# Kernel tuning notes

Hardware: AMD Instinct MI355X
Metric: run time of the kernel (lower is better)

Reference implementation:

```python
import jax, jax.numpy as jnp
import numpy as np

D_MODEL = 1024
NUM_HEADS = 16
D_K = D_MODEL // NUM_HEADS  # 64
THETA = 10000.0


def setup_inputs() -> dict:
    key = jax.random.key(0)
    k_x, k_q, k_k, k_v, k_o = jax.random.split(key, 5)
    B, S = 2, 2048
    std = (2.0 / (D_MODEL + D_MODEL)) ** 0.5
    x = jax.random.normal(k_x, (B, S, D_MODEL), dtype=jnp.float32)
    Wq = std * jax.random.truncated_normal(k_q, -3.0, 3.0, (D_MODEL, D_MODEL), dtype=jnp.float32)
    Wk = std * jax.random.truncated_normal(k_k, -3.0, 3.0, (D_MODEL, D_MODEL), dtype=jnp.float32)
    Wv = std * jax.random.truncated_normal(k_v, -3.0, 3.0, (D_MODEL, D_MODEL), dtype=jnp.float32)
    Wo = std * jax.random.truncated_normal(k_o, -3.0, 3.0, (D_MODEL, D_MODEL), dtype=jnp.float32)
    return {"x": x, "Wq": Wq, "Wk": Wk, "Wv": Wv, "Wo": Wo}


def _apply_rope(t, cos, sin):
    # t: [B, H, S, d_k]; cos/sin: [S, d_k//2] broadcast over B, H
    tr = t.reshape(*t.shape[:-1], D_K // 2, 2)
    t1, t2 = tr[..., 0], tr[..., 1]
    r1 = t1 * cos - t2 * sin
    r2 = t1 * sin + t2 * cos
    return jnp.stack([r1, r2], axis=-1).reshape(t.shape)


def reference(x, Wq, Wk, Wv, Wo):
    B, S, D = x.shape
    H, dk = NUM_HEADS, D_K
    # projections (no bias): y = x @ W.T
    Q = (x @ Wq.T).reshape(B, S, H, dk).transpose(0, 2, 1, 3)  # [B,H,S,dk]
    K = (x @ Wk.T).reshape(B, S, H, dk).transpose(0, 2, 1, 3)
    V = (x @ Wv.T).reshape(B, S, H, dk).transpose(0, 2, 1, 3)
    # RoPE angles for positions 0..S-1
    pos = jnp.arange(S, dtype=jnp.float32)[:, None]            # [S,1]
    freqs = 1.0 / (THETA ** (jnp.arange(0, dk, 2, dtype=jnp.float32) / dk))  # [dk/2]
    angles = pos * freqs[None, :]                              # [S, dk/2]
    cos, sin = jnp.cos(angles), jnp.sin(angles)
    Q = _apply_rope(Q, cos, sin)
    K = _apply_rope(K, cos, sin)
    # causal scaled dot-product attention
    scores = jnp.einsum("bhqd,bhkd->bhqk", Q, K) / jnp.sqrt(jnp.float32(dk))
    causal = jnp.tril(jnp.ones((S, S), dtype=bool))
    scores = jnp.where(causal, scores, -jnp.inf)
    probs = jax.nn.softmax(scores, axis=-1)
    attn = jnp.einsum("bhqk,bhkd->bhqd", probs, V)             # [B,H,S,dk]
    attn = attn.transpose(0, 2, 1, 3).reshape(B, S, H * dk)
    return attn @ Wo.T
```

## Files before the change

### kernel.cpp

```cpp
#include <hip/hip_runtime.h>
#include <hip/hip_bf16.h>

typedef __bf16 bf16;
typedef __bf16 bf16x8 __attribute__((ext_vector_type(8)));
typedef float f32x4 __attribute__((ext_vector_type(4)));

#define MFMA16(A, B, C) __builtin_amdgcn_mfma_f32_16x16x32_bf16((A), (B), (C), 0, 0, 0)

static __device__ __forceinline__ void gload16(const bf16* g, bf16* l) {
    __builtin_amdgcn_global_load_lds((const __attribute__((address_space(1))) void*)g,
                                     (__attribute__((address_space(3))) void*)l, 16, 0, 0);
}

__global__ void detect_kernel(const void* w, int* flag) {
    float v = (float)((const bf16*)w)[threadIdx.x];
    unsigned long long bad = __ballot(!(fabsf(v) < 1.0f));
    if (threadIdx.x == 0) *flag = bad ? 1 : 0;
}

__global__ __launch_bounds__(256) void convert_all(const void* x, const void* w0,
                                                   const void* w1, const void* w2,
                                                   const void* w3, bf16* xb, bf16* b0,
                                                   bf16* b1, bf16* b2, bf16* b3,
                                                   const int* flagp) {
    if (*flagp == 0) return;
    int id = (blockIdx.x * 256 + threadIdx.x) * 4;
    const int XN = 1 << 22;
    const float* src;
    bf16* dst;
    int off;
    if (id < XN) {
        src = (const float*)x; dst = xb; off = id;
    } else {
        int r = id - XN;
        int wi = r >> 20;
        off = r & ((1 << 20) - 1);
        src = (const float*)(wi == 0 ? w0 : wi == 1 ? w1 : wi == 2 ? w2 : w3);
        dst = (wi == 0 ? b0 : wi == 1 ? b1 : wi == 2 ? b2 : b3);
    }
    float4 v = *(const float4*)(src + off);
    bf16 o[4] = {(bf16)v.x, (bf16)v.y, (bf16)v.z, (bf16)v.w};
    *(uint2*)(dst + off) = *(uint2*)o;
}

template <int MODE>
__global__ __launch_bounds__(256, 3) void gemm_nt(const void* rawA, const bf16* convA,
                                                  const void* rW0, const bf16* cW0,
                                                  const void* rW1, const bf16* cW1,
                                                  const void* rW2, const bf16* cW2,
                                                  bf16* Qo, bf16* Ko, bf16* Vt,
                                                  float* p0, float* p1,
                                                  const int* flagp) {
    const int K = 1024;
    __shared__ __attribute__((aligned(16))) bf16 lsA[2][128 * 32];
    __shared__ __attribute__((aligned(16))) bf16 lsB[2][128 * 32];
    const int flag = *flagp;
    const bf16* A = flag ? convA : (const bf16*)rawA;
    int tensor, n0, m0, ks;
    const bf16* W;
    if (MODE == 0) {
        tensor = blockIdx.x >> 3;
        n0 = (blockIdx.x & 7) * 128;
        m0 = blockIdx.y * 128;
        ks = 0;
        W = tensor == 0 ? (flag ? cW0 : (const bf16*)rW0)
          : tensor == 1 ? (flag ? cW1 : (const bf16*)rW1)
                        : (flag ? cW2 : (const bf16*)rW2);
    } else {
        const int bid = blockIdx.x;
        ks = bid & 1;
        const int slot = bid >> 1;
        m0 = (slot & 31) * 128;
        n0 = (slot >> 5) * 128;
        tensor = 0;
        W = flag ? cW0 : (const bf16*)rW0;
    }
    const int t = threadIdx.x;
    const int w = t >> 6, lane = t & 63;
    const int wr = w >> 1, wc = w & 1;
    const int llo = lane & 15, quad = lane >> 4;
    const int sel = (llo >> 1) & 3;

    f32x4 acc[4][4] = {};

    auto stage = [&](int k0, int buf) {
#pragma unroll
        for (int j = 0; j < 2; ++j) {
            int c = j * 256 + t;
            int row = c >> 2, pos = c & 3;
            int g = pos ^ ((row >> 1) & 3);
            gload16(A + (size_t)(m0 + row) * K + k0 + g * 8, &lsA[buf][c * 8]);
        }
#pragma unroll
        for (int j = 0; j < 2; ++j) {
            int c = j * 256 + t;
            int row = c >> 2, pos = c & 3;
            int g = pos ^ ((row >> 1) & 3);
            gload16(W + (size_t)(n0 + row) * K + k0 + g * 8, &lsB[buf][c * 8]);
        }
    };

    auto compute = [&](int buf) {
        bf16x8 a[4], bb[4];
#pragma unroll
        for (int mi = 0; mi < 4; ++mi) {
            int r = wr * 64 + mi * 16 + llo;
            a[mi] = *(const bf16x8*)&lsA[buf][r * 32 + ((quad ^ sel) * 8)];
        }
#pragma unroll
        for (int ni = 0; ni < 4; ++ni) {
            int r = wc * 64 + ni * 16 + llo;
            bb[ni] = *(const bf16x8*)&lsB[buf][r * 32 + ((quad ^ sel) * 8)];
        }
#pragma unroll
        for (int mi = 0; mi < 4; ++mi)
#pragma unroll
            for (int ni = 0; ni < 4; ++ni)
                acc[mi][ni] = MFMA16(a[mi], bb[ni], acc[mi][ni]);
    };

    const int kbase = (MODE == 1) ? ks * 512 : 0;
    const int NIT = (MODE == 1) ? 16 : 32;

    stage(kbase, 0);
    for (int it = 0; it < NIT; it += 2) {
        __syncthreads();
        stage(kbase + (it + 1) * 32, 1);
        compute(0);
        __syncthreads();
        if (it + 2 < NIT) stage(kbase + (it + 2) * 32, 0);
        compute(1);
    }

#pragma unroll
    for (int mi = 0; mi < 4; ++mi)
#pragma unroll
        for (int ni = 0; ni < 4; ++ni)
#pragma unroll
            for (int r = 0; r < 4; ++r) {
                int row = m0 + wr * 64 + mi * 16 + quad * 4 + r;
                int col = n0 + wc * 64 + ni * 16 + llo;
                float v = acc[mi][ni][r];
                if (MODE == 1) {
                    float* dst = ks ? p1 : p0;
                    dst[(size_t)row * 1024 + col] = v;
                } else if (tensor == 2) {
                    int b = row >> 11, s = row & 2047;
                    Vt[((size_t)b * 1024 + col) * 2048 + s] = (bf16)v;
                } else {
                    int d = col & 63, s = row & 2047;
                    float partner = __shfl_xor(v, 1);
                    float freq = exp2f((float)(d >> 1) * -0.4152410118609203f);
                    float rev = (float)s * freq * 0.15915494309189535f;
                    rev -= floorf(rev);
                    float sn = __builtin_amdgcn_sinf(rev);
                    float cs = __builtin_amdgcn_cosf(rev);
                    float outv = v * cs + partner * sn * ((d & 1) ? 1.0f : -1.0f);
                    bf16* dst = (tensor == 0) ? Qo : Ko;
                    dst[(size_t)row * 1024 + col] = (bf16)outv;
                }
            }
}

__global__ __launch_bounds__(256) void reduce_out(const float* p0, const float* p1,
                                                  void* dout, const int* flagp) {
    int i = (blockIdx.x * 256 + threadIdx.x) * 4;
    float4 a = *(const float4*)(p0 + i);
    float4 b = *(const float4*)(p1 + i);
    float4 s = {a.x + b.x, a.y + b.y, a.z + b.z, a.w + b.w};
    if (*flagp) {
        *(float4*)((float*)dout + i) = s;
    } else {
        bf16 o[4] = {(bf16)s.x, (bf16)s.y, (bf16)s.z, (bf16)s.w};
        *(uint2*)((bf16*)dout + i) = *(uint2*)o;
    }
}

__global__ __launch_bounds__(256, 3) void attn_kernel(const bf16* __restrict__ Q,
                                                      const bf16* __restrict__ Kr,
                                                      const bf16* __restrict__ Vt,
                                                      bf16* __restrict__ O,
                                                      bf16* __restrict__ Opart,
                                                      float* __restrict__ lws) {
    __shared__ __attribute__((aligned(16))) bf16 lsK[2][64 * 64];
    __shared__ __attribute__((aligned(16))) bf16 lsV[2][64 * 64];
    __shared__ __attribute__((aligned(16))) bf16 lsP[4][32 * 64];
    const int blk = blockIdx.x;
    int ib, bh, s, tt0, tt1;
    bool split;
    if (blk < 512) {
        split = true;
        s = blk >> 8;
        int c = blk & 255;
        ib = 15 - (c >> 5);
        bh = c & 31;
        tt0 = s ? (ib + 1) : 0;
        tt1 = s ? (2 * ib + 1) : ib;
    } else {
        split = false;
        s = 0;
        int c = blk - 512;
        ib = c >> 5;
        bh = c & 31;
        tt0 = 0;
        tt1 = 2 * ib + 1;
    }
    const int b = bh >> 4, h = bh & 15;
    const int t = threadIdx.x, w = t >> 6, lane = t & 63;
    const int llo = lane & 15, quad = lane >> 4;
    const int q0w = ib * 128 + w * 32;

    bf16x8 aQ[2][2];
#pragma unroll
    for (int qi = 0; qi < 2; ++qi) {
        const size_t qb =
            ((size_t)(b * 2048 + q0w + qi * 16 + llo)) * 1024 + h * 64 + quad * 8;
        aQ[qi][0] = *(const bf16x8*)&Q[qb];
        aQ[qi][1] = *(const bf16x8*)&Q[qb + 32];
    }

    f32x4 o[2][4] = {};
    float lpart[2] = {0.f, 0.f};
    const float SC = 0.18033688011112042f;
    const int qlane0 = q0w + llo;

    const int srow8 = lane >> 3;
    const int sc = (lane & 7) ^ srow8;

    auto stage = [&](int tt, int buf) {
        const int kv0 = tt * 64;
#pragma unroll
        for (int jj = 0; jj < 2; ++jj) {
            int seg = w + jj * 4;
            int rowk = seg * 8 + srow8;
            gload16(&Kr[((size_t)(b * 2048 + kv0 + rowk)) * 1024 + h * 64 + sc * 8],
                    &lsK[buf][seg * 512 + lane * 8]);
            gload16(&Vt[((size_t)(b * 1024 + h * 64 + rowk)) * 2048 + kv0 + sc * 8],
                    &lsV[buf][seg * 512 + lane * 8]);
        }
    };

    stage(tt0, 0);

    for (int tt = tt0; tt <= tt1; ++tt) {
        const int cur = (tt - tt0) & 1;
        const int kv0 = tt * 64;
        __syncthreads();
        if (tt + 1 <= tt1) stage(tt + 1, cur ^ 1);

        if (kv0 <= q0w + 31) {
            bf16x8 kf[4][2];
#pragma unroll
            for (int half = 0; half < 4; ++half) {
                int rk = half * 16 + llo;
                kf[half][0] = *(const bf16x8*)&lsK[cur][rk * 64 + ((quad ^ (rk & 7)) * 8)];
                kf[half][1] =
                    *(const bf16x8*)&lsK[cur][rk * 64 + (((quad + 4) ^ (rk & 7)) * 8)];
            }
            bf16x8 vf[2][4];
#pragma unroll
            for (int kc = 0; kc < 2; ++kc)
#pragma unroll
                for (int g = 0; g < 4; ++g) {
                    int rv = g * 16 + llo;
                    int cg = kc * 4 + quad;
                    vf[kc][g] =
                        *(const bf16x8*)&lsV[cur][rv * 64 + ((cg ^ (rv & 7)) * 8)];
                }

            const bool need_mask = (kv0 + 63 >= q0w);
#pragma unroll
            for (int qi = 0; qi < 2; ++qi) {
                const int q = qlane0 + qi * 16;
                const int prow = qi * 16 + llo;
#pragma unroll
                for (int half = 0; half < 4; ++half) {
                    f32x4 z = {};
                    z = MFMA16(kf[half][0], aQ[qi][0], z);
                    z = MFMA16(kf[half][1], aQ[qi][1], z);
                    union { bf16 hh[4]; uint2 uu; } pk;
                    if (need_mask) {
                        int kvb = kv0 + half * 16 + quad * 4;
#pragma unroll
                        for (int r = 0; r < 4; ++r) {
                            float e = (kvb + r <= q) ? z[r] * SC : -INFINITY;
                            float p = __builtin_amdgcn_exp2f(e);
                            lpart[qi] += p;
                            pk.hh[r] = (bf16)p;
                        }
                    } else {
#pragma unroll
                        for (int r = 0; r < 4; ++r) {
                            float p = __builtin_amdgcn_exp2f(z[r] * SC);
                            lpart[qi] += p;
                            pk.hh[r] = (bf16)p;
                        }
                    }
                    int cw = 2 * half + (quad >> 1);
                    *(uint2*)&lsP[w][prow * 64 + ((cw ^ (llo & 7)) * 8) + (quad & 1) * 4] =
                        pk.uu;
                }
            }
            __builtin_amdgcn_wave_barrier();
#pragma unroll
            for (int qi = 0; qi < 2; ++qi) {
                const int prow = qi * 16 + llo;
#pragma unroll
                for (int kc = 0; kc < 2; ++kc) {
                    int cr = 4 * kc + quad;
                    bf16x8 aP =
                        *(const bf16x8*)&lsP[w][prow * 64 + ((cr ^ (llo & 7)) * 8)];
#pragma unroll
                    for (int g = 0; g < 4; ++g) o[qi][g] = MFMA16(aP, vf[kc][g], o[qi][g]);
                }
            }
            __builtin_amdgcn_wave_barrier();
        }
    }

    float lfull[2];
#pragma unroll
    for (int qi = 0; qi < 2; ++qi) {
        float l = lpart[qi];
        l += __shfl_xor(l, 16);
        l += __shfl_xor(l, 32);
        lfull[qi] = l;
    }

    if (split) {
        const int slotw = ((ib - 8) * 32 + bh) * 2 + s;
        bf16* op = Opart + (size_t)slotw * 8192;
#pragma unroll
        for (int qi = 0; qi < 2; ++qi) {
#pragma unroll
            for (int r = 0; r < 4; ++r) {
                int row_in = w * 32 + qi * 16 + quad * 4 + r;
#pragma unroll
                for (int g = 0; g < 4; ++g)
                    op[row_in * 64 + g * 16 + llo] = (bf16)o[qi][g][r];
            }
            if (quad == 0) lws[slotw * 128 + w * 32 + qi * 16 + llo] = lfull[qi];
        }
    } else {
#pragma unroll
        for (int qi = 0; qi < 2; ++qi)
#pragma unroll
            for (int r = 0; r < 4; ++r) {
                float l = __shfl(lfull[qi], (lane & 48) | (quad * 4 + r));
                float inv = 1.f / l;
                int q = q0w + qi * 16 + quad * 4 + r;
                size_t ob = ((size_t)(b * 2048 + q)) * 1024 + h * 64;
#pragma unroll
                for (int g = 0; g < 4; ++g)
                    O[ob + g * 16 + llo] = (bf16)(o[qi][g][r] * inv);
            }
    }
}

__global__ __launch_bounds__(256) void combine_kernel(const bf16* __restrict__ Opart,
                                                      const float* __restrict__ lws,
                                                      bf16* __restrict__ AO) {
    int id = blockIdx.x * 256 + threadIdx.x;
    int d = id & 63;
    int h = (id >> 6) & 15;
    int qoff = (id >> 10) & 1023;
    int b = id >> 20;
    int ib8 = qoff >> 7;
    int q_in = qoff & 127;
    int slot = (ib8 * 32 + (b * 16 + h)) * 2;
    size_t base = (size_t)slot * 8192 + q_in * 64 + d;
    float o0 = (float)Opart[base];
    float o1 = (float)Opart[base + 8192];
    float l = lws[slot * 128 + q_in] + lws[(slot + 1) * 128 + q_in];
    int q = 1024 + qoff;
    AO[((size_t)(b * 2048 + q)) * 1024 + h * 64 + d] = (bf16)((o0 + o1) / l);
}

extern "C" void kernel_launch(void* const* d_in, const int* in_sizes, int n_in,
                              void* d_out, int out_size, void* d_ws, size_t ws_size,
                              hipStream_t stream) {
    const size_t TN = (size_t)4096 * 1024;

    int* flag = (int*)d_ws;
    bf16* Q = (bf16*)((char*)d_ws + 256);
    bf16* Kb = Q + TN;
    bf16* Vt = Kb + TN;
    bf16* xb = Vt + TN;
    bf16* Wb0 = xb + TN;
    bf16* Wb1 = Wb0 + TN / 4;
    bf16* Wb2 = Wb1 + TN / 4;
    bf16* Wb3 = Wb2 + TN / 4;
    bf16* AO = Q;
    bf16* Opart = xb;
    float* lws = (float*)Wb0;
    float* p0 = (float*)Kb;
    float* p1 = (float*)xb;

    detect_kernel<<<1, 64, 0, stream>>>(d_in[1], flag);
    convert_all<<<8192, 256, 0, stream>>>(d_in[0], d_in[1], d_in[2], d_in[3], d_in[4],
                                          xb, Wb0, Wb1, Wb2, Wb3, flag);

    gemm_nt<0><<<dim3(24, 32), 256, 0, stream>>>(d_in[0], xb, d_in[1], Wb0, d_in[2],
                                                 Wb1, d_in[3], Wb2, Q, Kb, Vt, nullptr,
                                                 nullptr, flag);

    attn_kernel<<<768, 256, 0, stream>>>(Q, Kb, Vt, AO, Opart, lws);
    combine_kernel<<<8192, 256, 0, stream>>>(Opart, lws, AO);

    gemm_nt<1><<<512, 256, 0, stream>>>(AO, AO, d_in[4], Wb3, nullptr, nullptr,
                                        nullptr, nullptr, nullptr, nullptr, nullptr,
                                        p0, p1, flag);
    reduce_out<<<4096, 256, 0, stream>>>(p0, p1, d_out, flag);
}
```

Measured before the change: 194.2 us.

## Replace QKV projection GEMM with 256x256-tile, 512-thread, triple-buffered kernel

Adds a dedicated QKV projection kernel that uses 256x256 output tiles per 512-thread block, a three-slot LDS pipeline with two stages of prefetch, and a block-index swizzle for L2 locality. It fuses RoPE into the epilogue and writes V transposed. The goal is more data reuse per LDS load and better overlap of global loads with MFMA work. The cost is a large accumulator footprint (128 floats per thread) and only 192 blocks, which may underfill the GPU's CUs and limit occupancy.

```diff
diff --git a/kernel.cpp b/kernel.cpp
--- a/kernel.cpp
+++ b/kernel.cpp
@@ -41,6 +41,120 @@
     float4 v = *(const float4*)(src + off);
     bf16 o[4] = {(bf16)v.x, (bf16)v.y, (bf16)v.z, (bf16)v.w};
     *(uint2*)(dst + off) = *(uint2*)o;
+}
+
+__global__ __launch_bounds__(512, 2) void qkv_gemm(const void* rawA, const bf16* convA,
+                                                   const void* rW0, const bf16* cW0,
+                                                   const void* rW1, const bf16* cW1,
+                                                   const void* rW2, const bf16* cW2,
+                                                   bf16* Qo, bf16* Ko, bf16* Vt,
+                                                   const int* flagp) {
+    const int K = 1024;
+    const int NS = 32;
+    __shared__ __attribute__((aligned(16))) bf16 lsA[3][256 * 32];
+    __shared__ __attribute__((aligned(16))) bf16 lsB[3][256 * 32];
+    const int flag = *flagp;
+    const bf16* A = flag ? convA : (const bf16*)rawA;
+
+    const int swz = (blockIdx.x & 7) * 24 + (blockIdx.x >> 3);
+    const int m0 = (swz / 12) * 256;
+    const int bxn = swz % 12;
+    const int tensor = bxn >> 2;
+    const int n0 = (bxn & 3) * 256;
+    const bf16* W = tensor == 0 ? (flag ? cW0 : (const bf16*)rW0)
+                  : tensor == 1 ? (flag ? cW1 : (const bf16*)rW1)
+                                : (flag ? cW2 : (const bf16*)rW2);
+
+    const int t = threadIdx.x;
+    const int w = t >> 6, lane = t & 63;
+    const int wr = w >> 2, wc = w & 3;
+    const int llo = lane & 15, quad = lane >> 4;
+    const int sel = (llo >> 1) & 3;
+
+    f32x4 acc[8][4] = {};
+
+    auto stage = [&](int s, int slot) {
+#pragma unroll
+        for (int j = 0; j < 2; ++j) {
+            int c = j * 512 + t;
+            int row = c >> 2, pos = c & 3;
+            int g = pos ^ ((row >> 1) & 3);
+            gload16(A + (size_t)(m0 + row) * K + s * 32 + g * 8, &lsA[slot][c * 8]);
+        }
+#pragma unroll
+        for (int j = 0; j < 2; ++j) {
+            int c = j * 512 + t;
+            int row = c >> 2, pos = c & 3;
+            int g = pos ^ ((row >> 1) & 3);
+            gload16(W + (size_t)(n0 + row) * K + s * 32 + g * 8, &lsB[slot][c * 8]);
+        }
+    };
+
+    stage(0, 0);
+    stage(1, 1);
+    asm volatile("s_waitcnt vmcnt(4)" ::: "memory");
+    __builtin_amdgcn_s_barrier();
+    __builtin_amdgcn_sched_barrier(0);
+
+    int cur = 0;
+    for (int it = 0; it < NS; ++it) {
+        bf16x8 a[8], bb[4];
+#pragma unroll
+        for (int mi = 0; mi < 8; ++mi) {
+            int r = wr * 128 + mi * 16 + llo;
+            a[mi] = *(const bf16x8*)&lsA[cur][r * 32 + ((quad ^ sel) * 8)];
+        }
+#pragma unroll
+        for (int ni = 0; ni < 4; ++ni) {
+            int r = wc * 64 + ni * 16 + llo;
+            bb[ni] = *(const bf16x8*)&lsB[cur][r * 32 + ((quad ^ sel) * 8)];
+        }
+        if (it + 2 < NS) {
+            int ns = cur + 2;
+            if (ns >= 3) ns -= 3;
+            stage(it + 2, ns);
+        }
+#pragma unroll
+        for (int mi = 0; mi < 8; ++mi)
+#pragma unroll
+            for (int ni = 0; ni < 4; ++ni)
+                acc[mi][ni] = MFMA16(a[mi], bb[ni], acc[mi][ni]);
+        if (it < NS - 2) {
+            asm volatile("s_waitcnt vmcnt(4)" ::: "memory");
+        } else {
+            asm volatile("s_waitcnt vmcnt(0)" ::: "memory");
+        }
+        __builtin_amdgcn_s_barrier();
+        __builtin_amdgcn_sched_barrier(0);
+        cur = cur + 1;
+        if (cur >= 3) cur = 0;
+    }
+
+#pragma unroll
+    for (int mi = 0; mi < 8; ++mi)
+#pragma unroll
+        for (int ni = 0; ni < 4; ++ni)
+#pragma unroll
+            for (int r = 0; r < 4; ++r) {
+                int row = m0 + wr * 128 + mi * 16 + quad * 4 + r;
+                int col = n0 + wc * 64 + ni * 16 + llo;
+                float v = acc[mi][ni][r];
+                if (tensor == 2) {
+                    int b = row >> 11, srow = row & 2047;
+                    Vt[((size_t)b * 1024 + col) * 2048 + srow] = (bf16)v;
+                } else {
+                    int d = col & 63, srow = row & 2047;
+                    float partner = __shfl_xor(v, 1);
+                    float freq = exp2f((float)(d >> 1) * -0.4152410118609203f);
+                    float rev = (float)srow * freq * 0.15915494309189535f;
+                    rev -= floorf(rev);
+                    float sn = __builtin_amdgcn_sinf(rev);
+                    float cs = __builtin_amdgcn_cosf(rev);
+                    float outv = v * cs + partner * sn * ((d & 1) ? 1.0f : -1.0f);
+                    bf16* dst = (tensor == 0) ? Qo : Ko;
+                    dst[(size_t)row * 1024 + col] = (bf16)outv;
+                }
+            }
 }
 
 template <int MODE>
@@ -400,9 +514,8 @@
     convert_all<<<8192, 256, 0, stream>>>(d_in[0], d_in[1], d_in[2], d_in[3], d_in[4],
                                           xb, Wb0, Wb1, Wb2, Wb3, flag);
 
-    gemm_nt<0><<<dim3(24, 32), 256, 0, stream>>>(d_in[0], xb, d_in[1], Wb0, d_in[2],
-                                                 Wb1, d_in[3], Wb2, Q, Kb, Vt, nullptr,
-                                                 nullptr, flag);
+    qkv_gemm<<<192, 512, 0, stream>>>(d_in[0], xb, d_in[1], Wb0, d_in[2], Wb1,
+                                      d_in[3], Wb2, Q, Kb, Vt, flag);
 
     attn_kernel<<<768, 256, 0, stream>>>(Q, Kb, Vt, AO, Opart, lws);
     combine_kernel<<<8192, 256, 0, stream>>>(Opart, lws, AO);
```

After: 202.6 us. 1.04x slower.
